# Performance work log

Hardware: AMD Instinct MI355X
Metric: run time of the kernel (lower is better)

Reference implementation:

```python
import jax, jax.numpy as jnp
import numpy as np

NQ = 4  # n_qubits == hidden_dim

CNOT = jnp.array([[1,0,0,0],[0,1,0,0],[0,0,0,1],[0,0,1,0]], jnp.complex64)

def _ry_mat(theta):
    c = jnp.cos(theta / 2).astype(jnp.complex64)
    s = jnp.sin(theta / 2).astype(jnp.complex64)
    return jnp.stack([jnp.stack([c, -s], -1), jnp.stack([s, c], -1)], -2)

def _rx_mat(theta):
    c = jnp.cos(theta / 2).astype(jnp.complex64)
    s = jnp.sin(theta / 2).astype(jnp.complex64)
    js = (-1j) * s
    return jnp.stack([jnp.stack([c, js], -1), jnp.stack([js, c], -1)], -2)

def _rz_mat(theta):
    e = jnp.exp(-1j * theta.astype(jnp.complex64) / 2)
    z = jnp.zeros_like(e)
    return jnp.stack([jnp.stack([e, z], -1), jnp.stack([z, jnp.conj(e)], -1)], -2)

def _crx_mat(theta):
    c = jnp.cos(theta / 2).astype(jnp.complex64)
    s = ((-1j) * jnp.sin(theta / 2)).astype(jnp.complex64)
    m = jnp.zeros((4, 4), jnp.complex64)
    m = m.at[0, 0].set(1.0).at[1, 1].set(1.0)
    m = m.at[2, 2].set(c).at[2, 3].set(s).at[3, 2].set(s).at[3, 3].set(c)
    return m

def _apply1q(state, mat, wire):
    # state: (B, 2,2,2,2); mat: (2,2) shared or (B,2,2) batched
    s = jnp.moveaxis(state, 1 + wire, -1)
    if mat.ndim == 3:
        s = jnp.einsum('b...j,bij->b...i', s, mat)
    else:
        s = jnp.einsum('...j,ij->...i', s, mat)
    return jnp.moveaxis(s, -1, 1 + wire)

def _apply2q(state, mat, w0, w1):
    s = jnp.moveaxis(state, (1 + w0, 1 + w1), (-2, -1))
    sh = s.shape
    s = s.reshape(sh[:-2] + (4,))
    s = jnp.einsum('...j,ij->...i', s, mat)
    return jnp.moveaxis(s.reshape(sh), (-2, -1), (1 + w0, 1 + w1))

def _rand_ops(seed):
    # fixed random circuit emulating tq.RandomLayer(n_ops=20)
    rng = np.random.RandomState(seed)
    ops = []
    for _ in range(20):
        k = int(rng.randint(4))
        if k < 3:
            ops.append((k, int(rng.randint(NQ)), float(rng.uniform(0, 2 * np.pi))))
        else:
            w0 = int(rng.randint(NQ))
            w1 = int((w0 + 1 + rng.randint(NQ - 1)) % NQ)
            ops.append((3, (w0, w1), 0.0))
    return ops

RAND_OPS = [_rand_ops(s) for s in range(4)]  # one per gate layer (f,i,g,o)

def _qgate(angles, rx_p, ry_p, rz_p, crx_p, ops):
    # angles: (B, NQ) encoding angles; *_p: (NQ,) trainable scalars
    B = angles.shape[0]
    state = jnp.zeros((B, 2 ** NQ), jnp.complex64).at[:, 0].set(1.0)
    state = state.reshape((B,) + (2,) * NQ)
    for w in range(NQ):  # RY angle encoding
        state = _apply1q(state, _ry_mat(angles[:, w]), w)
    for k, w, t in ops:  # fixed random layer
        th = jnp.float32(t)
        if k == 0:
            state = _apply1q(state, _rx_mat(th), w)
        elif k == 1:
            state = _apply1q(state, _ry_mat(th), w)
        elif k == 2:
            state = _apply1q(state, _rz_mat(th), w)
        else:
            state = _apply2q(state, CNOT, w[0], w[1])
    for w in range(NQ):  # trainable ring
        state = _apply1q(state, _rx_mat(rx_p[w]), w)
        state = _apply1q(state, _ry_mat(ry_p[w]), w)
        state = _apply1q(state, _rz_mat(rz_p[w]), w)
        state = _apply2q(state, _crx_mat(crx_p[w]), w, (w + 1) % NQ)
    probs = jnp.abs(state) ** 2
    zs = []
    for w in range(NQ):  # <Z_w> = P(0) - P(1)
        p = jnp.moveaxis(probs, 1 + w, 1).reshape(B, 2, -1).sum(-1)
        zs.append(p[:, 0] - p[:, 1])
    return jnp.stack(zs, -1)  # (B, NQ)


def setup_inputs() -> dict:
    key = jax.random.key(0)
    ks = jax.random.split(key, 10)
    S, B, V, E, T = 256, 512, 128000, 256, 64
    D = E + NQ
    return {
        'sentence': jax.random.randint(ks[0], (S, B), 0, V),
        'emb': jax.random.normal(ks[1], (V, E), jnp.float32),
        'lin_w': jax.random.normal(ks[2], (4, NQ, D), jnp.float32) / np.sqrt(D),
        'lin_b': jax.random.normal(ks[3], (4, NQ), jnp.float32) * 0.1,
        'qrx': jax.random.normal(ks[4], (4, NQ), jnp.float32),
        'qry': jax.random.normal(ks[5], (4, NQ), jnp.float32),
        'qrz': jax.random.normal(ks[6], (4, NQ), jnp.float32),
        'qcrx': jax.random.normal(ks[7], (4, NQ), jnp.float32),
        'tag_w': jax.random.normal(ks[8], (T, NQ), jnp.float32) / np.sqrt(NQ),
        'tag_b': jax.random.normal(ks[9], (T,), jnp.float32) * 0.1,
    }


def reference(sentence, emb, lin_w, lin_b, qrx, qry, qrz, qcrx, tag_w, tag_b):
    embeds = emb[sentence]  # (S, B, E) embedding gather
    B = sentence.shape[1]
    h0 = jnp.zeros((B, NQ), jnp.float32)
    c0 = jnp.zeros((B, NQ), jnp.float32)

    def step(carry, x):
        hx, cx = carry
        comb = jnp.concatenate([x, hx], axis=-1)  # (B, E+NQ)
        ang = jnp.einsum('gqd,bd->gbq', lin_w, comb) + lin_b[:, None, :]
        f = jax.nn.sigmoid(_qgate(ang[0], qrx[0], qry[0], qrz[0], qcrx[0], RAND_OPS[0]))
        i = jax.nn.sigmoid(_qgate(ang[1], qrx[1], qry[1], qrz[1], qcrx[1], RAND_OPS[1]))
        g = jnp.tanh(_qgate(ang[2], qrx[2], qry[2], qrz[2], qcrx[2], RAND_OPS[2]))
        o = jax.nn.sigmoid(_qgate(ang[3], qrx[3], qry[3], qrz[3], qcrx[3], RAND_OPS[3]))
        cx = f * cx + i * g
        hx = o * jnp.tanh(cx)
        return (hx, cx), hx

    _, outs = jax.lax.scan(step, (h0, c0), embeds)  # (S, B, NQ)
    logits = jnp.einsum('sbh,th->sbt', outs, tag_w) + tag_b
    return jax.nn.log_softmax(logits, axis=-1)
```

## Files before the change

### kernel.cpp

```cpp
#include <hip/hip_runtime.h>
#include <math.h>

#define S_LEN 256
#define BATCH 512
#define ROWS (S_LEN * BATCH)
#define VOCAB 128000

struct MTState {
    unsigned mt[624];
    int idx;
    constexpr MTState(unsigned seed) : mt{}, idx(624) {
        mt[0] = seed;
        for (int i = 1; i < 624; ++i)
            mt[i] = 1812433253u * (mt[i - 1] ^ (mt[i - 1] >> 30)) + (unsigned)i;
    }
    constexpr unsigned next() {
        if (idx >= 624) {
            for (int i = 0; i < 624; ++i) {
                unsigned y = (mt[i] & 0x80000000u) | (mt[(i + 1) % 624] & 0x7fffffffu);
                mt[i] = mt[(i + 397) % 624] ^ (y >> 1) ^ ((y & 1u) ? 2567483615u : 0u);
            }
            idx = 0;
        }
        unsigned y = mt[idx++];
        y ^= y >> 11;
        y ^= (y << 7)  & 2636928640u;
        y ^= (y << 15) & 4022730752u;
        y ^= y >> 18;
        return y;
    }
};

struct OpsTab {
    int   k [4][20];
    int   w0[4][20];
    int   w1[4][20];
    float t [4][20];
};

constexpr OpsTab make_ops() {
    OpsTab o{};
    for (int seed = 0; seed < 4; ++seed) {
        MTState rng((unsigned)seed);
        for (int i = 0; i < 20; ++i) {
            unsigned k = rng.next() & 3u;
            if (k < 3u) {
                int w = (int)(rng.next() & 3u);
                unsigned A = rng.next(), B = rng.next();
                double d = ((double)(A >> 5) * 67108864.0 + (double)(B >> 6))
                           / 9007199254740992.0;
                o.k[seed][i]  = (int)k;
                o.w0[seed][i] = w;
                o.w1[seed][i] = 0;
                o.t[seed][i]  = (float)(6.283185307179586 * d);
            } else {
                int w0 = (int)(rng.next() & 3u);
                unsigned v = rng.next() & 3u;
                while (v > 2u) v = rng.next() & 3u;
                o.k[seed][i]  = 3;
                o.w0[seed][i] = w0;
                o.w1[seed][i] = (int)((w0 + 1 + (int)v) & 3);
                o.t[seed][i]  = 0.f;
            }
        }
    }
    return o;
}

__constant__ OpsTab OPS = make_ops();

__device__ inline float pfac(int t, int bj, int bk) {
    if (bj == bk)
        return (t == 0) ? 0.5f : (t == 1) ? (bj ? -0.5f : 0.5f) : 0.f;
    return (t == 2) ? 0.5f : 0.f;
}

__global__ __launch_bounds__(1024) void setup_kernel(const float* __restrict__ qrx,
                                                     const float* __restrict__ qry,
                                                     const float* __restrict__ qrz,
                                                     const float* __restrict__ qcrx,
                                                     float* __restrict__ Tg) {
    __shared__ float Mr[4 * 256];
    __shared__ float Mi[4 * 256];
    __shared__ float Q[16 * 256];

    int tid = threadIdx.x;
    int wv  = tid >> 6;
    int l   = tid & 63;
    int g   = wv >> 2;
    int r   = l & 15;
    int col = (wv & 3) * 4 + (l >> 4);

    float ar = (r == col) ? 1.f : 0.f;
    float ai = 0.f;
    int lbase = l & 48;

    for (int o = 0; o < 20; ++o) {
        int   k  = OPS.k[g][o];
        int   w  = OPS.w0[g][o];
        float th = OPS.t[g][o];
        if (k == 3) {
            int M1  = 8 >> OPS.w1[g][o];
            int M0  = 8 >> w;
            int src = lbase | (r ^ M1);
            float br = __shfl(ar, src, 64);
            float bi = __shfl(ai, src, 64);
            bool ctrl = (r & M0) != 0;
            ar = ctrl ? br : ar;
            ai = ctrl ? bi : ai;
        } else {
            int M = 8 >> w;
            float c = cosf(0.5f * th), s = sinf(0.5f * th);
            bool hi = (r & M) != 0;
            float Ar = c, Ai = 0.f, Br = 0.f, Bi = 0.f;
            if (k == 0) { Bi = -s; }
            else if (k == 1) { Br = hi ? s : -s; }
            else { Ai = hi ? s : -s; }
            int src = lbase | (r ^ M);
            float br = __shfl(ar, src, 64);
            float bi = __shfl(ai, src, 64);
            float nr = Ar * ar - Ai * ai + Br * br - Bi * bi;
            float ni = Ar * ai + Ai * ar + Br * bi + Bi * br;
            ar = nr; ai = ni;
        }
    }

    for (int w = 0; w < 4; ++w) {
        int M  = 8 >> w;
        int M1 = 8 >> ((w + 1) & 3);
        bool hi = (r & M) != 0;
        int src = lbase | (r ^ M);
        float th, c, s, br, bi, nr, ni;

        th = qrx[g * 4 + w]; c = cosf(0.5f * th); s = sinf(0.5f * th);
        br = __shfl(ar, src, 64); bi = __shfl(ai, src, 64);
        nr = c * ar + s * bi;  ni = c * ai - s * br;
        ar = nr; ai = ni;

        th = qry[g * 4 + w]; c = cosf(0.5f * th); s = sinf(0.5f * th);
        br = __shfl(ar, src, 64); bi = __shfl(ai, src, 64);
        { float B = hi ? s : -s;
          nr = c * ar + B * br;  ni = c * ai + B * bi; }
        ar = nr; ai = ni;

        th = qrz[g * 4 + w]; c = cosf(0.5f * th); s = sinf(0.5f * th);
        { float Ai2 = hi ? s : -s;
          nr = c * ar - Ai2 * ai;  ni = c * ai + Ai2 * ar; }
        ar = nr; ai = ni;

        th = qcrx[g * 4 + w]; c = cosf(0.5f * th); s = sinf(0.5f * th);
        int src1 = lbase | (r ^ M1);
        br = __shfl(ar, src1, 64); bi = __shfl(ai, src1, 64);
        bool ctrl = hi;
        nr = c * ar + s * bi;  ni = c * ai - s * br;
        ar = ctrl ? nr : ar;
        ai = ctrl ? ni : ai;
    }

    Mr[g * 256 + r * 16 + col] = ar;
    Mi[g * 256 + r * 16 + col] = ai;
    __syncthreads();

    for (int n = 0; n < 4; ++n) {
        int i  = tid * 4 + n;
        int gw = i >> 8, j = (i >> 4) & 15, kk = i & 15;
        int gg2 = gw >> 2, w = gw & 3;
        float acc = 0.f;
        for (int rr = 0; rr < 16; ++rr) {
            float sgn = ((rr >> (3 - w)) & 1) ? -1.f : 1.f;
            float mrj = Mr[gg2 * 256 + rr * 16 + j], mrk = Mr[gg2 * 256 + rr * 16 + kk];
            float mij = Mi[gg2 * 256 + rr * 16 + j], mik = Mi[gg2 * 256 + rr * 16 + kk];
            acc += sgn * (mrj * mrk + mij * mik);
        }
        Q[gw * 256 + j * 16 + kk] = acc;
    }
    __syncthreads();

    if (tid < 144) {
        int gw = tid / 9, rem = tid % 9, t0 = rem / 3, t1 = rem % 3;
        float acc[3][3] = {};
        for (int jk = 0; jk < 256; ++jk) {
            int j = jk >> 4, kq = jk & 15;
            int bj0 = (j >> 3) & 1, bk0 = (kq >> 3) & 1;
            int bj1 = (j >> 2) & 1, bk1 = (kq >> 2) & 1;
            int bj2 = (j >> 1) & 1, bk2 = (kq >> 1) & 1;
            int bj3 = j & 1,        bk3 = kq & 1;
            float f01 = pfac(t0, bj0, bk0) * pfac(t1, bj1, bk1);
            float base = Q[gw * 256 + jk] * f01;
#pragma unroll
            for (int t2 = 0; t2 < 3; ++t2) {
                float f2 = pfac(t2, bj2, bk2);
#pragma unroll
                for (int t3 = 0; t3 < 3; ++t3) {
                    float f3 = pfac(t3, bj3, bk3);
                    acc[t2][t3] = fmaf(base, f2 * f3, acc[t2][t3]);
                }
            }
        }
#pragma unroll
        for (int t2 = 0; t2 < 3; ++t2)
#pragma unroll
            for (int t3 = 0; t3 < 3; ++t3)
                Tg[gw * 81 + t0 * 27 + t1 * 9 + t2 * 3 + t3] = acc[t2][t3];
    }
}

#define TROWS 16
#define CH_STR 68
#define ROW_STR (4 * CH_STR)

__global__ __launch_bounds__(256) void proj_kernel(const float* __restrict__ emb,
                                                   const float* __restrict__ lin_w,
                                                   const float* __restrict__ lin_b,
                                                   float* __restrict__ proj) {
    __shared__ float lds[TROWS * ROW_STR];

    int tid = threadIdx.x;
    int l   = tid & 63;
    int q   = l & 15;
    int ch  = l >> 4;
    int wv  = tid >> 6;

    const float* wr = lin_w + q * 260 + ch * 64;
    float w0[16], w1[16], w2[16], w3[16];
#pragma unroll
    for (int j = 0; j < 16; ++j) {
        float4 t = *(const float4*)(wr + j * 4);
        w0[j] = t.x; w1[j] = t.y; w2[j] = t.z; w3[j] = t.w;
    }
    float bias = lin_b[q];

    const int ntiles = VOCAB / TROWS;
    for (int tile = blockIdx.x; tile < ntiles; tile += gridDim.x) {
        const float4* src = (const float4*)(emb + (size_t)tile * TROWS * 256);
#pragma unroll
        for (int i = 0; i < 4; ++i) {
            int f4  = tid + i * 256;
            int row = f4 >> 6;
            int c   = f4 & 63;
            float4 v = src[f4];
            *(float4*)(lds + row * ROW_STR + (c >> 4) * CH_STR + (c & 15) * 4) = v;
        }
        __syncthreads();

#pragma unroll
        for (int j = 0; j < 4; ++j) {
            int row = wv * 4 + j;
            const float* rp = lds + row * ROW_STR + ch * CH_STR;
            float acc = 0.f;
#pragma unroll
            for (int jj = 0; jj < 16; ++jj) {
                float4 x = *(const float4*)(rp + jj * 4);
                acc = fmaf(x.x, w0[jj], acc);
                acc = fmaf(x.y, w1[jj], acc);
                acc = fmaf(x.z, w2[jj], acc);
                acc = fmaf(x.w, w3[jj], acc);
            }
            acc += __shfl_xor(acc, 16, 64);
            acc += __shfl_xor(acc, 32, 64);
            if (l < 16) proj[(size_t)(tile * TROWS + row) * 16 + q] = acc + bias;
        }
        __syncthreads();
    }
}

__device__ inline float fast_sig(float k, float x) {
    return __builtin_amdgcn_rcpf(1.f + __expf(-k * x));
}

__global__ __launch_bounds__(64)
__attribute__((amdgpu_waves_per_eu(1, 1)))
void lstm_kernel(const float* __restrict__ lin_w,
                 const float* __restrict__ Tg,
                 const int* __restrict__ sent,
                 const float* __restrict__ proj,
                 float* __restrict__ outs) {
    int l = threadIdx.x;
    int g = l & 3;
    int w = (l >> 2) & 3;
    int q = l >> 4;
    int b = blockIdx.x * 4 + q;

    float T[81];
#pragma unroll
    for (int i = 0; i < 81; ++i) T[i] = Tg[(g * 4 + w) * 81 + i];

    float whp[4][4];
#pragma unroll
    for (int qq = 0; qq < 4; ++qq)
#pragma unroll
        for (int k = 0; k < 4; ++k)
            whp[qq][k] = lin_w[(g * 4 + qq) * 260 + 256 + ((w - k) & 3)];

    const float kk = (g == 2) ? 2.f : 1.f;
    const float sc = (g == 2) ? 2.f : 1.f;
    const float of = (g == 2) ? 1.f : 0.f;

    float hr0 = 0.f, hr1 = 0.f, hr2 = 0.f, hr3 = 0.f, cst = 0.f;

    const int* sp = sent + b;
    float* op = outs + (size_t)b * 4 + w;

    auto tokat = [&](int sidx) { return sp[(size_t)(sidx & 255) * BATCH]; };
    auto rowat = [&](int tok)  { return *(const float4*)(proj + (size_t)tok * 16 + g * 4); };

    int tk0 = tokat(4), tk1 = tokat(5), tk2 = tokat(6), tk3 = tokat(7);
    float4 A0 = rowat(tokat(0));
    float4 A1 = rowat(tokat(1));
    float4 A2 = rowat(tokat(2));
    float4 A3 = rowat(tokat(3));

    auto step = [&](float4 ax, int sidx) {
        float a0 = fmaf(whp[0][3], hr3, fmaf(whp[0][2], hr2, fmaf(whp[0][1], hr1, fmaf(whp[0][0], hr0, ax.x))));
        float a1 = fmaf(whp[1][3], hr3, fmaf(whp[1][2], hr2, fmaf(whp[1][1], hr1, fmaf(whp[1][0], hr0, ax.y))));
        float a2 = fmaf(whp[2][3], hr3, fmaf(whp[2][2], hr2, fmaf(whp[2][1], hr1, fmaf(whp[2][0], hr0, ax.z))));
        float a3 = fmaf(whp[3][3], hr3, fmaf(whp[3][2], hr2, fmaf(whp[3][1], hr1, fmaf(whp[3][0], hr0, ax.w))));

        float c0, s0, c1, s1, c2, s2, c3, s3;
        __sincosf(a0, &s0, &c0);
        __sincosf(a1, &s1, &c1);
        __sincosf(a2, &s2, &c2);
        __sincosf(a3, &s3, &c3);

        float yA[27];
#pragma unroll
        for (int i = 0; i < 27; ++i)
            yA[i] = fmaf(s3, T[i * 3 + 2], fmaf(c3, T[i * 3 + 1], T[i * 3]));
        float yB[9];
#pragma unroll
        for (int i = 0; i < 9; ++i)
            yB[i] = fmaf(s2, yA[i * 3 + 2], fmaf(c2, yA[i * 3 + 1], yA[i * 3]));
        float yC[3];
#pragma unroll
        for (int i = 0; i < 3; ++i)
            yC[i] = fmaf(s1, yB[i * 3 + 2], fmaf(c1, yB[i * 3 + 1], yB[i * 3]));
        float Z = fmaf(s0, yC[2], fmaf(c0, yC[1], yC[0]));

        float act = fmaf(sc, fast_sig(kk, Z), -of);

        int ai2 = __float_as_int(act);
        float f  = __int_as_float(__builtin_amdgcn_update_dpp(0, ai2, 0x00, 0xf, 0xf, true));
        float ii = __int_as_float(__builtin_amdgcn_update_dpp(0, ai2, 0x55, 0xf, 0xf, true));
        float gg = __int_as_float(__builtin_amdgcn_update_dpp(0, ai2, 0xAA, 0xf, 0xf, true));
        float oo = __int_as_float(__builtin_amdgcn_update_dpp(0, ai2, 0xFF, 0xf, 0xf, true));

        cst = fmaf(f, cst, ii * gg);
        float tn = fmaf(2.f, fast_sig(2.f, cst), -1.f);
        float hme = oo * tn;

        if (g == 0) op[(size_t)sidx * 2048] = hme;

        int hi = __float_as_int(hme);
        hr0 = hme;
        hr1 = __int_as_float(__builtin_amdgcn_update_dpp(hi, hi, 0x124, 0xf, 0xf, false));
        hr2 = __int_as_float(__builtin_amdgcn_update_dpp(hi, hi, 0x128, 0xf, 0xf, false));
        hr3 = __int_as_float(__builtin_amdgcn_update_dpp(hi, hi, 0x12C, 0xf, 0xf, false));
    };

    for (int s = 0; s < S_LEN; s += 4) {
        step(A0, s);     A0 = rowat(tk0); tk0 = tokat(s + 8);
        step(A1, s + 1); A1 = rowat(tk1); tk1 = tokat(s + 9);
        step(A2, s + 2); A2 = rowat(tk2); tk2 = tokat(s + 10);
        step(A3, s + 3); A3 = rowat(tk3); tk3 = tokat(s + 11);
    }
}

__global__ __launch_bounds__(256) void logits_kernel(const float* __restrict__ outs,
                                                     const float* __restrict__ tag_w,
                                                     const float* __restrict__ tag_b,
                                                     float* __restrict__ out) {
    int l = threadIdx.x & 63;
    int wid = (blockIdx.x * blockDim.x + threadIdx.x) >> 6;
    int nw  = (gridDim.x * blockDim.x) >> 6;

    float4 w = *(const float4*)(tag_w + l * 4);
    float bb = tag_b[l];

    for (int row = wid; row < ROWS; row += nw) {
        float4 h = *(const float4*)(outs + (size_t)row * 4);
        float z = fmaf(h.x, w.x, fmaf(h.y, w.y, fmaf(h.z, w.z, fmaf(h.w, w.w, bb))));
        float m = z;
#pragma unroll
        for (int d = 1; d < 64; d <<= 1) m = fmaxf(m, __shfl_xor(m, d, 64));
        float e = __expf(z - m);
        float ssum = e;
#pragma unroll
        for (int d = 1; d < 64; d <<= 1) ssum += __shfl_xor(ssum, d, 64);
        out[(size_t)row * 64 + l] = (z - m) - __logf(ssum);
    }
}

extern "C" void kernel_launch(void* const* d_in, const int* in_sizes, int n_in,
                              void* d_out, int out_size, void* d_ws, size_t ws_size,
                              hipStream_t stream) {
    const int*   sent  = (const int*)d_in[0];
    const float* emb   = (const float*)d_in[1];
    const float* lin_w = (const float*)d_in[2];
    const float* lin_b = (const float*)d_in[3];
    const float* qrx   = (const float*)d_in[4];
    const float* qry   = (const float*)d_in[5];
    const float* qrz   = (const float*)d_in[6];
    const float* qcrx  = (const float*)d_in[7];
    const float* tag_w = (const float*)d_in[8];
    const float* tag_b = (const float*)d_in[9];
    float* out = (float*)d_out;

    char* ws = (char*)d_ws;
    float*  Tg   = (float*)ws;
    float*  proj = (float*)(ws + 8192);
    float*  outs = (float*)(ws + 8192 + (size_t)VOCAB * 16 * 4);

    setup_kernel<<<dim3(1), dim3(1024), 0, stream>>>(qrx, qry, qrz, qcrx, Tg);
    proj_kernel<<<dim3(2048), dim3(256), 0, stream>>>(emb, lin_w, lin_b, proj);
    lstm_kernel<<<dim3(128), dim3(64), 0, stream>>>(lin_w, Tg, sent, proj, outs);
    logits_kernel<<<dim3(1024), dim3(256), 0, stream>>>(outs, tag_w, tag_b, out);
}
```

Before: 204.9 us.

## Rework projection, interleave two LSTM batches per wave, vectorize logits softmax

The projection kernel stops staging embedding tiles in shared memory. Each wave now reads rows straight from global memory, computes four output channels per lane, and reduces with shuffles, which removes the barriers. The LSTM kernel runs two independent batch chains in each wave and halves the grid, so there is more instruction-level parallelism to hide latency on the serial recurrence, at the cost of higher register pressure. The logits kernel processes 16 rows per wave with 16 tags per lane and vectorized stores, replacing the per-row full-wave shuffle reductions.

Result: slower. 284.2 us (+38.7%).

```diff
diff --git a/kernel.cpp b/kernel.cpp
--- a/kernel.cpp
+++ b/kernel.cpp
@@ -205,62 +205,61 @@
     }
 }
 
-#define TROWS 16
-#define CH_STR 68
-#define ROW_STR (4 * CH_STR)
-
 __global__ __launch_bounds__(256) void proj_kernel(const float* __restrict__ emb,
                                                    const float* __restrict__ lin_w,
                                                    const float* __restrict__ lin_b,
                                                    float* __restrict__ proj) {
-    __shared__ float lds[TROWS * ROW_STR];
-
     int tid = threadIdx.x;
     int l   = tid & 63;
-    int q   = l & 15;
-    int ch  = l >> 4;
     int wv  = tid >> 6;
-
-    const float* wr = lin_w + q * 260 + ch * 64;
-    float w0[16], w1[16], w2[16], w3[16];
-#pragma unroll
-    for (int j = 0; j < 16; ++j) {
-        float4 t = *(const float4*)(wr + j * 4);
-        w0[j] = t.x; w1[j] = t.y; w2[j] = t.z; w3[j] = t.w;
-    }
-    float bias = lin_b[q];
-
-    const int ntiles = VOCAB / TROWS;
+    int ch  = l & 15;
+    int rl  = l >> 4;
+
+    float wq[4][16];
+#pragma unroll
+    for (int qq = 0; qq < 4; ++qq) {
+        const float* wr = lin_w + (wv * 4 + qq) * 260 + ch * 16;
+#pragma unroll
+        for (int j = 0; j < 4; ++j) {
+            float4 t = *(const float4*)(wr + j * 4);
+            wq[qq][j * 4 + 0] = t.x; wq[qq][j * 4 + 1] = t.y;
+            wq[qq][j * 4 + 2] = t.z; wq[qq][j * 4 + 3] = t.w;
+        }
+    }
+    float4 bz = *(const float4*)(lin_b + wv * 4);
+
+    const int ntiles = VOCAB / 16;
     for (int tile = blockIdx.x; tile < ntiles; tile += gridDim.x) {
-        const float4* src = (const float4*)(emb + (size_t)tile * TROWS * 256);
-#pragma unroll
-        for (int i = 0; i < 4; ++i) {
-            int f4  = tid + i * 256;
-            int row = f4 >> 6;
-            int c   = f4 & 63;
-            float4 v = src[f4];
-            *(float4*)(lds + row * ROW_STR + (c >> 4) * CH_STR + (c & 15) * 4) = v;
-        }
-        __syncthreads();
-
-#pragma unroll
-        for (int j = 0; j < 4; ++j) {
-            int row = wv * 4 + j;
-            const float* rp = lds + row * ROW_STR + ch * CH_STR;
-            float acc = 0.f;
-#pragma unroll
-            for (int jj = 0; jj < 16; ++jj) {
-                float4 x = *(const float4*)(rp + jj * 4);
-                acc = fmaf(x.x, w0[jj], acc);
-                acc = fmaf(x.y, w1[jj], acc);
-                acc = fmaf(x.z, w2[jj], acc);
-                acc = fmaf(x.w, w3[jj], acc);
+        const float* base = emb + (size_t)tile * 16 * 256;
+#pragma unroll
+        for (int r4 = 0; r4 < 4; ++r4) {
+            const float* rp = base + (r4 * 4 + rl) * 256 + ch * 16;
+            float xs[16];
+            *(float4*)&xs[0]  = ((const float4*)rp)[0];
+            *(float4*)&xs[4]  = ((const float4*)rp)[1];
+            *(float4*)&xs[8]  = ((const float4*)rp)[2];
+            *(float4*)&xs[12] = ((const float4*)rp)[3];
+
+            float p[4] = {0.f, 0.f, 0.f, 0.f};
+#pragma unroll
+            for (int qq = 0; qq < 4; ++qq)
+#pragma unroll
+                for (int d = 0; d < 16; ++d)
+                    p[qq] = fmaf(xs[d], wq[qq][d], p[qq]);
+
+#pragma unroll
+            for (int d = 1; d < 16; d <<= 1) {
+                p[0] += __shfl_xor(p[0], d, 64);
+                p[1] += __shfl_xor(p[1], d, 64);
+                p[2] += __shfl_xor(p[2], d, 64);
+                p[3] += __shfl_xor(p[3], d, 64);
             }
-            acc += __shfl_xor(acc, 16, 64);
-            acc += __shfl_xor(acc, 32, 64);
-            if (l < 16) proj[(size_t)(tile * TROWS + row) * 16 + q] = acc + bias;
-        }
-        __syncthreads();
+            if (ch == 0) {
+                float4 o = make_float4(p[0] + bz.x, p[1] + bz.y,
+                                       p[2] + bz.z, p[3] + bz.w);
+                *(float4*)(proj + ((size_t)(tile * 16 + r4 * 4 + rl) * 16 + wv * 4)) = o;
+            }
+        }
     }
 }
 
@@ -279,7 +278,8 @@
     int g = l & 3;
     int w = (l >> 2) & 3;
     int q = l >> 4;
-    int b = blockIdx.x * 4 + q;
+    int ba = blockIdx.x * 8 + q;
+    int bb = ba + 4;
 
     float T[81];
 #pragma unroll
@@ -296,21 +296,25 @@
     const float sc = (g == 2) ? 2.f : 1.f;
     const float of = (g == 2) ? 1.f : 0.f;
 
-    float hr0 = 0.f, hr1 = 0.f, hr2 = 0.f, hr3 = 0.f, cst = 0.f;
-
-    const int* sp = sent + b;
-    float* op = outs + (size_t)b * 4 + w;
-
-    auto tokat = [&](int sidx) { return sp[(size_t)(sidx & 255) * BATCH]; };
-    auto rowat = [&](int tok)  { return *(const float4*)(proj + (size_t)tok * 16 + g * 4); };
-
-    int tk0 = tokat(4), tk1 = tokat(5), tk2 = tokat(6), tk3 = tokat(7);
-    float4 A0 = rowat(tokat(0));
-    float4 A1 = rowat(tokat(1));
-    float4 A2 = rowat(tokat(2));
-    float4 A3 = rowat(tokat(3));
-
-    auto step = [&](float4 ax, int sidx) {
+    float hr0a = 0.f, hr1a = 0.f, hr2a = 0.f, hr3a = 0.f, csta = 0.f;
+    float hr0b = 0.f, hr1b = 0.f, hr2b = 0.f, hr3b = 0.f, cstb = 0.f;
+
+    const int* spa = sent + ba;
+    const int* spb = sent + bb;
+    float* opa = outs + (size_t)ba * 4 + w;
+    float* opb = outs + (size_t)bb * 4 + w;
+
+    auto toka = [&](int sidx) { return spa[(size_t)(sidx & 255) * BATCH]; };
+    auto tokb = [&](int sidx) { return spb[(size_t)(sidx & 255) * BATCH]; };
+    auto rowat = [&](int tok) { return *(const float4*)(proj + (size_t)tok * 16 + g * 4); };
+
+    int tk0a = toka(4), tk1a = toka(5), tk2a = toka(6), tk3a = toka(7);
+    int tk0b = tokb(4), tk1b = tokb(5), tk2b = tokb(6), tk3b = tokb(7);
+    float4 A0a = rowat(toka(0)), A1a = rowat(toka(1)), A2a = rowat(toka(2)), A3a = rowat(toka(3));
+    float4 A0b = rowat(tokb(0)), A1b = rowat(tokb(1)), A2b = rowat(tokb(2)), A3b = rowat(tokb(3));
+
+    auto step = [&](float4 ax, float& hr0, float& hr1, float& hr2, float& hr3,
+                    float& cst) -> float {
         float a0 = fmaf(whp[0][3], hr3, fmaf(whp[0][2], hr2, fmaf(whp[0][1], hr1, fmaf(whp[0][0], hr0, ax.x))));
         float a1 = fmaf(whp[1][3], hr3, fmaf(whp[1][2], hr2, fmaf(whp[1][1], hr1, fmaf(whp[1][0], hr0, ax.y))));
         float a2 = fmaf(whp[2][3], hr3, fmaf(whp[2][2], hr2, fmaf(whp[2][1], hr1, fmaf(whp[2][0], hr0, ax.z))));
@@ -348,20 +352,39 @@
         float tn = fmaf(2.f, fast_sig(2.f, cst), -1.f);
         float hme = oo * tn;
 
-        if (g == 0) op[(size_t)sidx * 2048] = hme;
-
         int hi = __float_as_int(hme);
         hr0 = hme;
         hr1 = __int_as_float(__builtin_amdgcn_update_dpp(hi, hi, 0x124, 0xf, 0xf, false));
         hr2 = __int_as_float(__builtin_amdgcn_update_dpp(hi, hi, 0x128, 0xf, 0xf, false));
         hr3 = __int_as_float(__builtin_amdgcn_update_dpp(hi, hi, 0x12C, 0xf, 0xf, false));
+        return hme;
     };
 
     for (int s = 0; s < S_LEN; s += 4) {
-        step(A0, s);     A0 = rowat(tk0); tk0 = tokat(s + 8);
-        step(A1, s + 1); A1 = rowat(tk1); tk1 = tokat(s + 9);
-        step(A2, s + 2); A2 = rowat(tk2); tk2 = tokat(s + 10);
-        step(A3, s + 3); A3 = rowat(tk3); tk3 = tokat(s + 11);
+        float ha, hb;
+        ha = step(A0a, hr0a, hr1a, hr2a, hr3a, csta);
+        hb = step(A0b, hr0b, hr1b, hr2b, hr3b, cstb);
+        if (g == 0) { opa[(size_t)s * 2048] = ha; opb[(size_t)s * 2048] = hb; }
+        A0a = rowat(tk0a); tk0a = toka(s + 8);
+        A0b = rowat(tk0b); tk0b = tokb(s + 8);
+
+        ha = step(A1a, hr0a, hr1a, hr2a, hr3a, csta);
+        hb = step(A1b, hr0b, hr1b, hr2b, hr3b, cstb);
+        if (g == 0) { opa[(size_t)(s + 1) * 2048] = ha; opb[(size_t)(s + 1) * 2048] = hb; }
+        A1a = rowat(tk1a); tk1a = toka(s + 9);
+        A1b = rowat(tk1b); tk1b = tokb(s + 9);
+
+        ha = step(A2a, hr0a, hr1a, hr2a, hr3a, csta);
+        hb = step(A2b, hr0b, hr1b, hr2b, hr3b, cstb);
+        if (g == 0) { opa[(size_t)(s + 2) * 2048] = ha; opb[(size_t)(s + 2) * 2048] = hb; }
+        A2a = rowat(tk2a); tk2a = toka(s + 10);
+        A2b = rowat(tk2b); tk2b = tokb(s + 10);
+
+        ha = step(A3a, hr0a, hr1a, hr2a, hr3a, csta);
+        hb = step(A3b, hr0b, hr1b, hr2b, hr3b, cstb);
+        if (g == 0) { opa[(size_t)(s + 3) * 2048] = ha; opb[(size_t)(s + 3) * 2048] = hb; }
+        A3a = rowat(tk3a); tk3a = toka(s + 11);
+        A3b = rowat(tk3b); tk3b = tokb(s + 11);
     }
 }
 
@@ -369,24 +392,46 @@
                                                      const float* __restrict__ tag_w,
                                                      const float* __restrict__ tag_b,
                                                      float* __restrict__ out) {
-    int l = threadIdx.x & 63;
-    int wid = (blockIdx.x * blockDim.x + threadIdx.x) >> 6;
-    int nw  = (gridDim.x * blockDim.x) >> 6;
-
-    float4 w = *(const float4*)(tag_w + l * 4);
-    float bb = tag_b[l];
-
-    for (int row = wid; row < ROWS; row += nw) {
-        float4 h = *(const float4*)(outs + (size_t)row * 4);
-        float z = fmaf(h.x, w.x, fmaf(h.y, w.y, fmaf(h.z, w.z, fmaf(h.w, w.w, bb))));
-        float m = z;
-#pragma unroll
-        for (int d = 1; d < 64; d <<= 1) m = fmaxf(m, __shfl_xor(m, d, 64));
-        float e = __expf(z - m);
-        float ssum = e;
-#pragma unroll
-        for (int d = 1; d < 64; d <<= 1) ssum += __shfl_xor(ssum, d, 64);
-        out[(size_t)row * 64 + l] = (z - m) - __logf(ssum);
+    int tid = blockIdx.x * 256 + threadIdx.x;
+    int wid = tid >> 6;
+    int l   = threadIdx.x & 63;
+    int row = wid * 16 + (l >> 2);
+    int t0  = (l & 3) * 16;
+
+    float tw[16][4], tb[16];
+#pragma unroll
+    for (int t = 0; t < 16; ++t) {
+        float4 v = *(const float4*)(tag_w + (t0 + t) * 4);
+        tw[t][0] = v.x; tw[t][1] = v.y; tw[t][2] = v.z; tw[t][3] = v.w;
+        tb[t] = tag_b[t0 + t];
+    }
+
+    float4 h = *(const float4*)(outs + (size_t)row * 4);
+
+    float z[16];
+#pragma unroll
+    for (int t = 0; t < 16; ++t)
+        z[t] = fmaf(h.w, tw[t][3], fmaf(h.z, tw[t][2],
+                fmaf(h.y, tw[t][1], fmaf(h.x, tw[t][0], tb[t]))));
+
+    float m = z[0];
+#pragma unroll
+    for (int t = 1; t < 16; ++t) m = fmaxf(m, z[t]);
+    m = fmaxf(m, __shfl_xor(m, 1, 64));
+    m = fmaxf(m, __shfl_xor(m, 2, 64));
+
+    float e = 0.f;
+#pragma unroll
+    for (int t = 0; t < 16; ++t) e += __expf(z[t] - m);
+    e += __shfl_xor(e, 1, 64);
+    e += __shfl_xor(e, 2, 64);
+
+    float lg = m + __logf(e);
+    float* op = out + (size_t)row * 64 + t0;
+#pragma unroll
+    for (int t = 0; t < 16; t += 4) {
+        float4 o = make_float4(z[t] - lg, z[t + 1] - lg, z[t + 2] - lg, z[t + 3] - lg);
+        *(float4*)(op + t) = o;
     }
 }
 
@@ -412,6 +457,6 @@
 
     setup_kernel<<<dim3(1), dim3(1024), 0, stream>>>(qrx, qry, qrz, qcrx, Tg);
     proj_kernel<<<dim3(2048), dim3(256), 0, stream>>>(emb, lin_w, lin_b, proj);
-    lstm_kernel<<<dim3(128), dim3(64), 0, stream>>>(lin_w, Tg, sent, proj, outs);
-    logits_kernel<<<dim3(1024), dim3(256), 0, stream>>>(outs, tag_w, tag_b, out);
-}
+    lstm_kernel<<<dim3(64), dim3(64), 0, stream>>>(lin_w, Tg, sent, proj, outs);
+    logits_kernel<<<dim3(2048), dim3(256), 0, stream>>>(outs, tag_w, tag_b, out);
+}
```
